# Optimization experiments

Hardware: AMD Instinct MI355X
Metric: run time of the kernel (lower is better)

## Reference

```python
import jax, jax.numpy as jnp
import numpy as np

N = 100000   # nodes
E = 300000   # edges
D = 256      # emb_dim
L = 5        # num_layers
SELF_LOOP_BOND_TYPE = 4
BN_EPS = 1e-5


def setup_inputs() -> dict:
    key = jax.random.key(0)
    ks = jax.random.split(key, 12)
    s = 0.05
    x = jax.random.randint(ks[0], (N, 2), 0, 3)
    edge_index = jax.random.randint(ks[1], (2, E), 0, N)
    edge_attr = jax.random.randint(ks[2], (E, 2), 0, 3)
    x_emb1 = jax.random.normal(ks[3], (120, D), dtype=jnp.float32) * s
    x_emb2 = jax.random.normal(ks[4], (3, D), dtype=jnp.float32) * s
    edge_emb1 = jax.random.normal(ks[5], (L, 6, D), dtype=jnp.float32) * s
    edge_emb2 = jax.random.normal(ks[6], (L, 3, D), dtype=jnp.float32) * s
    W1 = jax.random.normal(ks[7], (L, D, 2 * D), dtype=jnp.float32) * (1.0 / np.sqrt(D))
    b1 = jnp.zeros((L, 2 * D), dtype=jnp.float32)
    W2 = jax.random.normal(ks[8], (L, 2 * D, D), dtype=jnp.float32) * (1.0 / np.sqrt(2 * D))
    b2 = jnp.zeros((L, D), dtype=jnp.float32)
    bn_gamma = jnp.ones((L - 1, D), dtype=jnp.float32)
    bn_beta = jnp.zeros((L - 1, D), dtype=jnp.float32)
    return dict(x=x, edge_index=edge_index, edge_attr=edge_attr,
                x_emb1=x_emb1, x_emb2=x_emb2,
                edge_emb1=edge_emb1, edge_emb2=edge_emb2,
                W1=W1, b1=b1, W2=W2, b2=b2,
                bn_gamma=bn_gamma, bn_beta=bn_beta)


def reference(x, edge_index, edge_attr, x_emb1, x_emb2, edge_emb1, edge_emb2,
              W1, b1, W2, b2, bn_gamma, bn_beta):
    n = x.shape[0]
    loop = jnp.arange(n)
    # add_self_loops: append (i, i) for every node
    src = jnp.concatenate([edge_index[0], loop])  # [E+N]
    dst = jnp.concatenate([edge_index[1], loop])  # [E+N]
    # self-loop edge_attr = (bond_type=4, direction=0)
    self_attr = jnp.concatenate([
        jnp.full((n, 1), SELF_LOOP_BOND_TYPE, dtype=edge_attr.dtype),
        jnp.zeros((n, 1), dtype=edge_attr.dtype)], axis=1)
    ea = jnp.concatenate([edge_attr, self_attr], axis=0)  # [E+N, 2]

    out = x_emb1[x[:, 0]] + x_emb2[x[:, 1]]  # [N, D]
    for l in range(L):
        e_emb = edge_emb1[l][ea[:, 0]] + edge_emb2[l][ea[:, 1]]  # [E+N, D]
        msg = out[src] + e_emb                                   # gather + message
        agg = jax.ops.segment_sum(msg, dst, num_segments=n)      # scatter-add
        h = jax.nn.relu(agg @ W1[l] + b1[l]) @ W2[l] + b2[l]     # GIN MLP
        if l < L - 1:
            mean = h.mean(axis=0)
            var = h.var(axis=0)  # biased var, matches torch BN training
            h = (h - mean) * jax.lax.rsqrt(var + BN_EPS) * bn_gamma[l] + bn_beta[l]
            h = jax.nn.relu(h)
        out = h
    return out
```

## Files before the change

### kernel.cpp

```cpp
#include <hip/hip_runtime.h>

typedef unsigned short u16;
typedef unsigned int u32;

#define DD 256

typedef short  s16x8 __attribute__((ext_vector_type(8)));
typedef short  s16x4 __attribute__((ext_vector_type(4)));
typedef float  f32x4 __attribute__((ext_vector_type(4)));

__device__ __forceinline__ float b2f(u16 u){
  union { u32 i; float f; } c; c.i = ((u32)u) << 16; return c.f;
}
__device__ __forceinline__ u16 f2b(float f){
  union { float f; u32 i; } c; c.f = f;
  u32 b = c.i + 0x7FFFu + ((c.i >> 16) & 1u);
  return (u16)(b >> 16);
}

__global__ void NodeEncoder_72971494359603_kernel(){}

__global__ void probe_dtype(const u32* w, u32* flag){
  if (threadIdx.x == 0 && blockIdx.x == 0){
    int cnt = 0;
    for (int i = 0; i < 256; i++){
      u32 low = w[i] & 0xFFFFu;
      u32 e = (low >> 7) & 0xFFu;
      if (e >= 0x60u && e <= 0x7Eu) cnt++;
    }
    *flag = (cnt >= 192) ? 1u : 0u;
  }
}

__global__ void cvt_in(const void* src, u16* dst, int n, const u32* flag){
  int i = blockIdx.x * 256 + threadIdx.x;
  if (i < n){
    if (*flag){
      dst[i] = ((const u16*)src)[i];
    } else {
      dst[i] = f2b(((const float*)src)[i]);
    }
  }
}

__global__ void store_out(const u16* h, void* dout, int n, const u32* flag){
  int i = blockIdx.x * 256 + threadIdx.x;
  if (i < n){
    if (*flag){
      ((u16*)dout)[i] = h[i];
    } else {
      ((float*)dout)[i] = b2f(h[i]);
    }
  }
}

__global__ void zero_int(int* p, int n){
  int i = blockIdx.x * 256 + threadIdx.x;
  if (i < n) p[i] = 0;
}

__global__ void build_table(const u16* ee1, const u16* ee2, float* TBL){
  int b = blockIdx.x;
  int l = b / 18, c = b % 18, a = c / 3, bb = c % 3;
  int j = threadIdx.x;
  TBL[b * DD + j] = b2f(ee1[(l * 6 + a) * DD + j]) + b2f(ee2[(l * 3 + bb) * DD + j]);
}

__global__ void hist_kernel(const int* dst, int* counts, int E){
  int e = blockIdx.x * 256 + threadIdx.x;
  if (e < E) atomicAdd(&counts[dst[e]], 1);
}

__global__ void scan_sums(const int* counts, int* bsum, int N){
  __shared__ int red[256];
  int tid = threadIdx.x;
  int base = blockIdx.x * 1024;
  int s = 0;
  for (int i = tid; i < 1024; i += 256){
    int g = base + i;
    if (g < N) s += counts[g];
  }
  red[tid] = s;
  __syncthreads();
  for (int off = 128; off > 0; off >>= 1){
    if (tid < off) red[tid] += red[tid + off];
    __syncthreads();
  }
  if (tid == 0) bsum[blockIdx.x] = red[0];
}

__global__ void scan_top(int* bsum, int nb){
  if (threadIdx.x == 0 && blockIdx.x == 0){
    int acc = 0;
    for (int i = 0; i < nb; i++){ int t = bsum[i]; bsum[i] = acc; acc += t; }
  }
}

__global__ void scan_block(const int* counts, const int* bsum,
                           int* offsets, int* cursor, int N){
  __shared__ int tsum[256];
  int b = blockIdx.x;
  int tid = threadIdx.x;
  int base = b * 1024;
  int v0, v1, v2, v3;
  int g = base + tid * 4;
  v0 = (g + 0 < N) ? counts[g + 0] : 0;
  v1 = (g + 1 < N) ? counts[g + 1] : 0;
  v2 = (g + 2 < N) ? counts[g + 2] : 0;
  v3 = (g + 3 < N) ? counts[g + 3] : 0;
  tsum[tid] = v0 + v1 + v2 + v3;
  __syncthreads();
  for (int off = 1; off < 256; off <<= 1){
    int t = (tid >= off) ? tsum[tid - off] : 0;
    __syncthreads();
    tsum[tid] += t;
    __syncthreads();
  }
  int excl = (tid == 0 ? 0 : tsum[tid - 1]) + bsum[b];
  if (g + 0 < N){ offsets[g + 0] = excl; cursor[g + 0] = excl; } excl += v0;
  if (g + 1 < N){ offsets[g + 1] = excl; cursor[g + 1] = excl; } excl += v1;
  if (g + 2 < N){ offsets[g + 2] = excl; cursor[g + 2] = excl; } excl += v2;
  if (g + 3 < N){ offsets[g + 3] = excl; cursor[g + 3] = excl; }
}

__global__ void fill_csr(const int* ei, const int* ea, int* cursor,
                         int* payload, int E){
  int e = blockIdx.x * 256 + threadIdx.x;
  if (e < E){
    int d = ei[E + e];
    int pos = atomicAdd(&cursor[d], 1);
    int a = ea[2 * e], bb = ea[2 * e + 1];
    payload[pos] = ei[e] | ((a * 3 + bb) << 17);
  }
}

__global__ void node_embed(const int* x, const u16* xe1, const u16* xe2,
                           u16* out, int N){
  int idx = blockIdx.x * 256 + threadIdx.x;
  if (idx < N * DD){
    int n = idx >> 8, j = idx & 255;
    int x0 = x[2 * n], x1 = x[2 * n + 1];
    out[idx] = f2b(b2f(xe1[x0 * DD + j]) + b2f(xe2[x1 * DD + j]));
  }
}

__global__ void aggregate(const u16* __restrict__ feat, const float* __restrict__ TBL,
                          const int* __restrict__ offsets, const int* __restrict__ counts,
                          const int* __restrict__ payload, u16* __restrict__ agg, int N,
                          const float* __restrict__ sums, const u16* __restrict__ gamma,
                          const u16* __restrict__ beta, float invN, int apply_bn){
  __shared__ __align__(16) float T[18 * DD];
  int tid = threadIdx.x;
  for (int i = tid; i < 18 * DD; i += 256) T[i] = TBL[i];
  __syncthreads();
  int wave = tid >> 6, lane = tid & 63;
  int c4 = lane * 4;
  float sc[4], sh[4];
  if (apply_bn){
#pragma unroll
    for (int e = 0; e < 4; e++){
      int j = c4 + e;
      float mean = sums[j] * invN;
      float var = sums[DD + j] * invN - mean * mean;
      if (var < 0.f) var = 0.f;
      float scl = rsqrtf(var + 1e-5f) * b2f(gamma[j]);
      sc[e] = scl; sh[e] = b2f(beta[j]) - mean * scl;
    }
  } else {
#pragma unroll
    for (int e = 0; e < 4; e++){ sc[e] = 1.f; sh[e] = 0.f; }
  }
  int n0 = blockIdx.x * 32 + wave * 8;
  for (int u = 0; u < 8; u++){
    int n = n0 + u;
    if (n >= N) return;
    s16x4 sv = *(const s16x4*)(feat + (size_t)n * DD + c4);
    f32x4 tb = *(const f32x4*)(T + 12 * DD + c4);
    float v0 = b2f((u16)sv[0]) * sc[0] + sh[0];
    float v1 = b2f((u16)sv[1]) * sc[1] + sh[1];
    float v2 = b2f((u16)sv[2]) * sc[2] + sh[2];
    float v3 = b2f((u16)sv[3]) * sc[3] + sh[3];
    if (apply_bn){
      v0 = fmaxf(v0, 0.f); v1 = fmaxf(v1, 0.f);
      v2 = fmaxf(v2, 0.f); v3 = fmaxf(v3, 0.f);
    }
    float a0 = v0 + tb[0], a1 = v1 + tb[1], a2 = v2 + tb[2], a3 = v3 + tb[3];
    int e0 = offsets[n], cnt = counts[n];
    for (int e = e0; e < e0 + cnt; e++){
      int pl = payload[e];
      int src = pl & 0x1FFFF;
      int idx = pl >> 17;
      s16x4 rv = *(const s16x4*)(feat + (size_t)src * DD + c4);
      f32x4 tv = *(const f32x4*)(T + idx * DD + c4);
      float w0 = b2f((u16)rv[0]) * sc[0] + sh[0];
      float w1 = b2f((u16)rv[1]) * sc[1] + sh[1];
      float w2 = b2f((u16)rv[2]) * sc[2] + sh[2];
      float w3 = b2f((u16)rv[3]) * sc[3] + sh[3];
      if (apply_bn){
        w0 = fmaxf(w0, 0.f); w1 = fmaxf(w1, 0.f);
        w2 = fmaxf(w2, 0.f); w3 = fmaxf(w3, 0.f);
      }
      a0 += w0 + tv[0];
      a1 += w1 + tv[1];
      a2 += w2 + tv[2];
      a3 += w3 + tv[3];
    }
    s16x4 o;
    o[0] = (short)f2b(a0); o[1] = (short)f2b(a1);
    o[2] = (short)f2b(a2); o[3] = (short)f2b(a3);
    *(s16x4*)(agg + (size_t)n * DD + c4) = o;
  }
}

__global__ void pack_B(const u16* __restrict__ W, u16* __restrict__ Wp, int K, int Nc){
  int idx = blockIdx.x * 256 + threadIdx.x;
  int lane = idx & 63;
  int t = idx >> 6;
  int nk = K >> 5;
  int ksub = t % nk, cblk = t / nk;
  if (cblk >= (Nc >> 4)) return;
  int col = cblk * 16 + (lane & 15);
  int krow = ksub * 32 + (lane >> 4) * 8;
  u16* dst = Wp + (size_t)idx * 8;
#pragma unroll
  for (int e = 0; e < 8; e++)
    dst[e] = W[(size_t)(krow + e) * Nc + col];
}

__global__ void mlp_fused(const u16* __restrict__ A, const u16* __restrict__ Wp1,
                          const u16* __restrict__ bias1, const u16* __restrict__ Wp2,
                          const u16* __restrict__ bias2, u16* __restrict__ H, int M){
  __shared__ __align__(16) u16 As[64 * 256];
  __shared__ __align__(16) u16 Ms[64 * 128];
  int tid = threadIdx.x;
  int lane = tid & 63;
  int wave = tid >> 6;
  int wr = wave >> 2, wc = wave & 3;
  int row0 = blockIdx.x * 64;
  int lrow = lane & 15;
  int lk8 = (lane >> 4) * 8;
  int r4 = (lane >> 4) * 4;

  int srow = tid >> 5, slot = tid & 31;
#pragma unroll
  for (int p = 0; p < 4; p++){
    int r = p * 16 + srow;
    int gr = row0 + r; if (gr > M - 1) gr = M - 1;
    s16x8 v = *(const s16x8*)(A + (size_t)gr * DD + slot * 8);
    int byteo = r * 512 + ((slot * 16) ^ ((r & 7) << 4));
    *(s16x8*)((char*)As + byteo) = v;
  }

  f32x4 zero = {0.f, 0.f, 0.f, 0.f};
  f32x4 acc2[2][4];
#pragma unroll
  for (int m = 0; m < 2; m++)
#pragma unroll
    for (int n = 0; n < 4; n++) acc2[m][n] = zero;

  __syncthreads();

  for (int c = 0; c < 4; c++){
    f32x4 acc1[2][2];
#pragma unroll
    for (int m = 0; m < 2; m++)
#pragma unroll
      for (int n = 0; n < 2; n++) acc1[m][n] = zero;
#pragma unroll
    for (int ks = 0; ks < 8; ks++){
      s16x8 af[2], bf[2];
#pragma unroll
      for (int m = 0; m < 2; m++){
        int arow = wr * 32 + m * 16 + lrow;
        int byteo = arow * 512 + (((ks * 32 + lk8) * 2) ^ ((arow & 7) << 4));
        af[m] = *(const s16x8*)((const char*)As + byteo);
      }
#pragma unroll
      for (int n = 0; n < 2; n++){
        int cb = c * 8 + wc * 2 + n;
        size_t fidx = ((size_t)cb * 8 + ks) * 64 + lane;
        bf[n] = *(const s16x8*)(Wp1 + fidx * 8);
      }
#pragma unroll
      for (int m = 0; m < 2; m++)
#pragma unroll
        for (int n = 0; n < 2; n++)
          acc1[m][n] = __builtin_amdgcn_mfma_f32_16x16x32_bf16(
              af[m], bf[n], acc1[m][n], 0, 0, 0);
    }
    __syncthreads();
#pragma unroll
    for (int n = 0; n < 2; n++){
      float bv = b2f(bias1[c * 128 + wc * 32 + n * 16 + lrow]);
      int colb = (wc * 32 + n * 16 + lrow) * 2;
#pragma unroll
      for (int m = 0; m < 2; m++){
#pragma unroll
        for (int r = 0; r < 4; r++){
          float v = acc1[m][n][r] + bv;
          if (v < 0.f) v = 0.f;
          int mrow = wr * 32 + m * 16 + r4 + r;
          int byteo = (mrow * 256 + colb) ^ ((mrow & 7) << 4);
          *(u16*)((char*)Ms + byteo) = f2b(v);
        }
      }
    }
    __syncthreads();
#pragma unroll
    for (int ks = 0; ks < 4; ks++){
      s16x8 mf[2], wf[4];
#pragma unroll
      for (int m = 0; m < 2; m++){
        int mrow = wr * 32 + m * 16 + lrow;
        int byteo = mrow * 256 + (((ks * 32 + lk8) * 2) ^ ((mrow & 7) << 4));
        mf[m] = *(const s16x8*)((const char*)Ms + byteo);
      }
#pragma unroll
      for (int n = 0; n < 4; n++){
        int cb2 = wc * 4 + n;
        size_t fidx = ((size_t)cb2 * 16 + c * 4 + ks) * 64 + lane;
        wf[n] = *(const s16x8*)(Wp2 + fidx * 8);
      }
#pragma unroll
      for (int m = 0; m < 2; m++)
#pragma unroll
        for (int n = 0; n < 4; n++)
          acc2[m][n] = __builtin_amdgcn_mfma_f32_16x16x32_bf16(
              mf[m], wf[n], acc2[m][n], 0, 0, 0);
    }
  }

  float bv2[4];
#pragma unroll
  for (int n = 0; n < 4; n++) bv2[n] = b2f(bias2[wc * 64 + n * 16 + lrow]);
#pragma unroll
  for (int m = 0; m < 2; m++){
    int rb = row0 + wr * 32 + m * 16 + r4;
#pragma unroll
    for (int r = 0; r < 4; r++){
      int row = rb + r;
      if (row >= M) continue;
      u16* cp = H + (size_t)row * DD + wc * 64 + lrow;
#pragma unroll
      for (int n = 0; n < 4; n++)
        cp[n * 16] = f2b(acc2[m][n][r] + bv2[n]);
    }
  }
}

#define SBLK 256
__global__ void bn_stats(const u16* __restrict__ h, float* __restrict__ partial,
                         int N, int rpb){
  __shared__ float redS[8][256];
  __shared__ float redQ[8][256];
  int t = threadIdx.x;
  int rl = t >> 5, cg = (t & 31) * 8;
  int r0 = blockIdx.x * rpb;
  int r1 = r0 + rpb; if (r1 > N) r1 = N;
  float s[8], q[8];
#pragma unroll
  for (int e = 0; e < 8; e++){ s[e] = 0.f; q[e] = 0.f; }
  for (int r = r0 + rl; r < r1; r += 8){
    s16x8 v = *(const s16x8*)(h + (size_t)r * DD + cg);
#pragma unroll
    for (int e = 0; e < 8; e++){
      float f = b2f((u16)v[e]);
      s[e] += f; q[e] += f * f;
    }
  }
#pragma unroll
  for (int e = 0; e < 8; e++){ redS[rl][cg + e] = s[e]; redQ[rl][cg + e] = q[e]; }
  __syncthreads();
  float a = 0.f, b = 0.f;
#pragma unroll
  for (int k = 0; k < 8; k++){ a += redS[k][t]; b += redQ[k][t]; }
  partial[(size_t)blockIdx.x * DD + t] = a;
  partial[(size_t)(SBLK + blockIdx.x) * DD + t] = b;
}

__global__ void bn_reduce(const float* __restrict__ partial, float* __restrict__ sums){
  int j = threadIdx.x;
  int which = blockIdx.x;
  float s = 0.f;
  for (int i = 0; i < SBLK; i++)
    s += partial[(size_t)(which * SBLK + i) * DD + j];
  sums[which * DD + j] = s;
}

extern "C" void kernel_launch(void* const* d_in, const int* in_sizes, int n_in,
                              void* d_out, int out_size, void* d_ws, size_t ws_size,
                              hipStream_t stream){
  (void)n_in; (void)out_size; (void)ws_size;
  const int* x    = (const int*)d_in[0];
  const int* ei   = (const int*)d_in[1];
  const int* ea   = (const int*)d_in[2];
  const void* xe1 = d_in[3];
  const void* xe2 = d_in[4];
  const void* ee1 = d_in[5];
  const void* ee2 = d_in[6];
  const void* W1  = d_in[7];
  const void* b1  = d_in[8];
  const void* W2  = d_in[9];
  const void* b2  = d_in[10];
  const void* gam = d_in[11];
  const void* bet = d_in[12];

  int N = in_sizes[0] / 2;
  int E = in_sizes[1] / 2;
  int NB = (N + 1023) / 1024;
  const int L = 5;

  char* base = (char*)d_ws;
  size_t off = 0;
  u32* flag    = (u32*)(base + off);   off += 256;
  float* TBL   = (float*)(base + off); off += ((size_t)L * 18 * DD * 4 + 255) & ~(size_t)255;
  int* counts  = (int*)(base + off);   off += ((size_t)N * 4 + 255) & ~(size_t)255;
  int* offsets = (int*)(base + off);   off += ((size_t)N * 4 + 255) & ~(size_t)255;
  int* cursor  = (int*)(base + off);   off += ((size_t)N * 4 + 255) & ~(size_t)255;
  int* bsum    = (int*)(base + off);   off += ((size_t)NB * 4 + 255) & ~(size_t)255;
  int* payload = (int*)(base + off);   off += ((size_t)E * 4 + 255) & ~(size_t)255;
  float* part  = (float*)(base + off); off += ((size_t)2 * SBLK * DD * 4 + 255) & ~(size_t)255;
  float* sums  = (float*)(base + off); off += ((size_t)2 * DD * 4 + 255) & ~(size_t)255;
  u16* wx1  = (u16*)(base + off); off += ((size_t)120 * DD * 2 + 255) & ~(size_t)255;
  u16* wx2  = (u16*)(base + off); off += ((size_t)3 * DD * 2 + 255) & ~(size_t)255;
  u16* wee1 = (u16*)(base + off); off += ((size_t)L * 6 * DD * 2 + 255) & ~(size_t)255;
  u16* wee2 = (u16*)(base + off); off += ((size_t)L * 3 * DD * 2 + 255) & ~(size_t)255;
  u16* wW1  = (u16*)(base + off); off += ((size_t)L * DD * 2 * DD * 2 + 255) & ~(size_t)255;
  u16* wb1  = (u16*)(base + off); off += ((size_t)L * 2 * DD * 2 + 255) & ~(size_t)255;
  u16* wW2  = (u16*)(base + off); off += ((size_t)L * 2 * DD * DD * 2 + 255) & ~(size_t)255;
  u16* wb2  = (u16*)(base + off); off += ((size_t)L * DD * 2 + 255) & ~(size_t)255;
  u16* wgam = (u16*)(base + off); off += ((size_t)(L - 1) * DD * 2 + 255) & ~(size_t)255;
  u16* wbet = (u16*)(base + off); off += ((size_t)(L - 1) * DD * 2 + 255) & ~(size_t)255;
  u16* Wp1  = (u16*)(base + off); off += ((size_t)L * DD * 2 * DD * 2 + 255) & ~(size_t)255;
  u16* Wp2  = (u16*)(base + off); off += ((size_t)L * 2 * DD * DD * 2 + 255) & ~(size_t)255;
  u16* feat = (u16*)(base + off); off += ((size_t)N * DD * 2 + 255) & ~(size_t)255;
  u16* agg  = (u16*)(base + off); off += ((size_t)N * DD * 2 + 255) & ~(size_t)255;

  probe_dtype<<<1, 64, 0, stream>>>((const u32*)xe1, flag);
  cvt_in<<<(120 * DD + 255) / 256, 256, 0, stream>>>(xe1, wx1, 120 * DD, flag);
  cvt_in<<<(3 * DD + 255) / 256, 256, 0, stream>>>(xe2, wx2, 3 * DD, flag);
  cvt_in<<<(L * 6 * DD + 255) / 256, 256, 0, stream>>>(ee1, wee1, L * 6 * DD, flag);
  cvt_in<<<(L * 3 * DD + 255) / 256, 256, 0, stream>>>(ee2, wee2, L * 3 * DD, flag);
  cvt_in<<<(L * DD * 2 * DD + 255) / 256, 256, 0, stream>>>(W1, wW1, L * DD * 2 * DD, flag);
  cvt_in<<<(L * 2 * DD + 255) / 256, 256, 0, stream>>>(b1, wb1, L * 2 * DD, flag);
  cvt_in<<<(L * 2 * DD * DD + 255) / 256, 256, 0, stream>>>(W2, wW2, L * 2 * DD * DD, flag);
  cvt_in<<<(L * DD + 255) / 256, 256, 0, stream>>>(b2, wb2, L * DD, flag);
  cvt_in<<<((L - 1) * DD + 255) / 256, 256, 0, stream>>>(gam, wgam, (L - 1) * DD, flag);
  cvt_in<<<((L - 1) * DD + 255) / 256, 256, 0, stream>>>(bet, wbet, (L - 1) * DD, flag);

  build_table<<<90, 256, 0, stream>>>(wee1, wee2, TBL);
  for (int l = 0; l < L; l++){
    pack_B<<<64, 256, 0, stream>>>(wW1 + (size_t)l * DD * 2 * DD,
                                   Wp1 + (size_t)l * DD * 2 * DD, DD, 2 * DD);
    pack_B<<<64, 256, 0, stream>>>(wW2 + (size_t)l * 2 * DD * DD,
                                   Wp2 + (size_t)l * 2 * DD * DD, 2 * DD, DD);
  }
  zero_int<<<(N + 255) / 256, 256, 0, stream>>>(counts, N);
  hist_kernel<<<(E + 255) / 256, 256, 0, stream>>>(ei + E, counts, E);
  scan_sums<<<NB, 256, 0, stream>>>(counts, bsum, N);
  scan_top<<<1, 64, 0, stream>>>(bsum, NB);
  scan_block<<<NB, 256, 0, stream>>>(counts, bsum, offsets, cursor, N);
  fill_csr<<<(E + 255) / 256, 256, 0, stream>>>(ei, ea, cursor, payload, E);

  node_embed<<<(N * DD + 255) / 256, 256, 0, stream>>>(x, wx1, wx2, feat, N);

  int rpb_s = (N + SBLK - 1) / SBLK;
  float invN = 1.0f / (float)N;

  for (int l = 0; l < L; l++){
    aggregate<<<(N + 31) / 32, 256, 0, stream>>>(
        feat, TBL + (size_t)l * 18 * DD, offsets, counts, payload, agg, N,
        sums, wgam + (size_t)(l > 0 ? l - 1 : 0) * DD,
        wbet + (size_t)(l > 0 ? l - 1 : 0) * DD, invN, l > 0 ? 1 : 0);

    mlp_fused<<<(N + 63) / 64, 512, 0, stream>>>(
        agg, Wp1 + (size_t)l * DD * 2 * DD, wb1 + (size_t)l * 2 * DD,
        Wp2 + (size_t)l * 2 * DD * DD, wb2 + (size_t)l * DD, feat, N);

    if (l < L - 1){
      bn_stats<<<SBLK, 256, 0, stream>>>(feat, part, N, rpb_s);
      bn_reduce<<<2, 256, 0, stream>>>(part, sums);
    }
  }

  store_out<<<(N * DD + 255) / 256, 256, 0, stream>>>(feat, d_out, N * DD, flag);
}
```

Baseline: 1.574 ms.

## Restructure fused MLP per-wave and fold BN statistics into its epilogue

The MLP kernel now gives each wave its own 32-row tile with private LDS, so the block-wide syncthreads disappear, and each wave computes all 256 output columns across 16 hidden chunks. The output is staged through LDS for coalesced 16-byte stores, and per-column sum and sum-of-squares partials are accumulated in the same pass. This removes the separate bn_stats kernel and its full re-read of the feature matrix. bn_reduce is widened to 16 blocks with shuffle reductions to handle the larger number of partials. The trade-off is a large accumulator footprint (128 fp32 per lane for acc2), lower occupancy, and weight fragments being re-fetched from global memory per wave without reuse across waves.

```diff
diff --git a/kernel.cpp b/kernel.cpp
--- a/kernel.cpp
+++ b/kernel.cpp
@@ -227,40 +227,36 @@
     dst[e] = W[(size_t)(krow + e) * Nc + col];
 }
 
-__global__ void mlp_fused(const u16* __restrict__ A, const u16* __restrict__ Wp1,
-                          const u16* __restrict__ bias1, const u16* __restrict__ Wp2,
-                          const u16* __restrict__ bias2, u16* __restrict__ H, int M){
-  __shared__ __align__(16) u16 As[64 * 256];
-  __shared__ __align__(16) u16 Ms[64 * 128];
-  int tid = threadIdx.x;
-  int lane = tid & 63;
-  int wave = tid >> 6;
-  int wr = wave >> 2, wc = wave & 3;
-  int row0 = blockIdx.x * 64;
-  int lrow = lane & 15;
-  int lk8 = (lane >> 4) * 8;
-  int r4 = (lane >> 4) * 4;
-
-  int srow = tid >> 5, slot = tid & 31;
-#pragma unroll
-  for (int p = 0; p < 4; p++){
-    int r = p * 16 + srow;
-    int gr = row0 + r; if (gr > M - 1) gr = M - 1;
-    s16x8 v = *(const s16x8*)(A + (size_t)gr * DD + slot * 8);
-    int byteo = r * 512 + ((slot * 16) ^ ((r & 7) << 4));
-    *(s16x8*)((char*)As + byteo) = v;
+__global__ __launch_bounds__(256, 2)
+void mlp_fused(const u16* __restrict__ A, const u16* __restrict__ Wp1,
+               const u16* __restrict__ bias1, const u16* __restrict__ Wp2,
+               const u16* __restrict__ bias2, u16* __restrict__ H,
+               float* __restrict__ partial, int npart, int M){
+  __shared__ __align__(16) u16 As[4 * 32 * 256];
+  __shared__ __align__(16) u16 Ms[4 * 32 * 64];
+  int tid = threadIdx.x, lane = tid & 63, wave = tid >> 6;
+  char* as = (char*)(As + wave * 32 * 256);
+  char* ms = (char*)(Ms + wave * 32 * 64);
+  int wrow0 = blockIdx.x * 128 + wave * 32;
+  int lr = lane & 15, hi = lane >> 4;
+
+#pragma unroll
+  for (int p = 0; p < 16; p++){
+    int lin = p * 64 + lane;
+    int r = lin >> 5, sl = lin & 31;
+    int gr = wrow0 + r; if (gr > M - 1) gr = M - 1;
+    s16x8 v = *(const s16x8*)(A + (size_t)gr * DD + sl * 8);
+    *(s16x8*)(as + r * 512 + ((sl << 4) ^ ((r & 7) << 4))) = v;
   }
 
   f32x4 zero = {0.f, 0.f, 0.f, 0.f};
-  f32x4 acc2[2][4];
+  f32x4 acc2[2][16];
 #pragma unroll
   for (int m = 0; m < 2; m++)
 #pragma unroll
-    for (int n = 0; n < 4; n++) acc2[m][n] = zero;
-
-  __syncthreads();
-
-  for (int c = 0; c < 4; c++){
+    for (int n = 0; n < 16; n++) acc2[m][n] = zero;
+
+  for (int cc = 0; cc < 16; cc++){
     f32x4 acc1[2][2];
 #pragma unroll
     for (int m = 0; m < 2; m++)
@@ -268,123 +264,114 @@
       for (int n = 0; n < 2; n++) acc1[m][n] = zero;
 #pragma unroll
     for (int ks = 0; ks < 8; ks++){
-      s16x8 af[2], bf[2];
+      s16x8 af[2];
 #pragma unroll
       for (int m = 0; m < 2; m++){
-        int arow = wr * 32 + m * 16 + lrow;
-        int byteo = arow * 512 + (((ks * 32 + lk8) * 2) ^ ((arow & 7) << 4));
-        af[m] = *(const s16x8*)((const char*)As + byteo);
+        int arow = m * 16 + lr;
+        af[m] = *(const s16x8*)(as + arow * 512 +
+                                ((ks * 64 + hi * 16) ^ ((arow & 7) << 4)));
       }
 #pragma unroll
       for (int n = 0; n < 2; n++){
-        int cb = c * 8 + wc * 2 + n;
-        size_t fidx = ((size_t)cb * 8 + ks) * 64 + lane;
-        bf[n] = *(const s16x8*)(Wp1 + fidx * 8);
-      }
-#pragma unroll
-      for (int m = 0; m < 2; m++)
-#pragma unroll
-        for (int n = 0; n < 2; n++)
-          acc1[m][n] = __builtin_amdgcn_mfma_f32_16x16x32_bf16(
-              af[m], bf[n], acc1[m][n], 0, 0, 0);
-    }
-    __syncthreads();
+        int cb = cc * 2 + n;
+        s16x8 bf = *(const s16x8*)(Wp1 + (((size_t)cb * 8 + ks) * 64 + lane) * 8);
+        acc1[0][n] = __builtin_amdgcn_mfma_f32_16x16x32_bf16(af[0], bf, acc1[0][n], 0, 0, 0);
+        acc1[1][n] = __builtin_amdgcn_mfma_f32_16x16x32_bf16(af[1], bf, acc1[1][n], 0, 0, 0);
+      }
+    }
 #pragma unroll
     for (int n = 0; n < 2; n++){
-      float bv = b2f(bias1[c * 128 + wc * 32 + n * 16 + lrow]);
-      int colb = (wc * 32 + n * 16 + lrow) * 2;
+      float bv = b2f(bias1[cc * 32 + n * 16 + lr]);
+      int c2 = (n * 16 + lr) * 2;
 #pragma unroll
       for (int m = 0; m < 2; m++){
 #pragma unroll
         for (int r = 0; r < 4; r++){
+          int mrow = m * 16 + hi * 4 + r;
           float v = acc1[m][n][r] + bv;
-          if (v < 0.f) v = 0.f;
-          int mrow = wr * 32 + m * 16 + r4 + r;
-          int byteo = (mrow * 256 + colb) ^ ((mrow & 7) << 4);
-          *(u16*)((char*)Ms + byteo) = f2b(v);
+          v = fmaxf(v, 0.f);
+          *(u16*)(ms + mrow * 128 + (c2 ^ ((mrow & 7) << 4))) = f2b(v);
         }
       }
     }
-    __syncthreads();
-#pragma unroll
-    for (int ks = 0; ks < 4; ks++){
-      s16x8 mf[2], wf[4];
-#pragma unroll
-      for (int m = 0; m < 2; m++){
-        int mrow = wr * 32 + m * 16 + lrow;
-        int byteo = mrow * 256 + (((ks * 32 + lk8) * 2) ^ ((mrow & 7) << 4));
-        mf[m] = *(const s16x8*)((const char*)Ms + byteo);
-      }
-#pragma unroll
-      for (int n = 0; n < 4; n++){
-        int cb2 = wc * 4 + n;
-        size_t fidx = ((size_t)cb2 * 16 + c * 4 + ks) * 64 + lane;
-        wf[n] = *(const s16x8*)(Wp2 + fidx * 8);
-      }
-#pragma unroll
-      for (int m = 0; m < 2; m++)
-#pragma unroll
-        for (int n = 0; n < 4; n++)
-          acc2[m][n] = __builtin_amdgcn_mfma_f32_16x16x32_bf16(
-              mf[m], wf[n], acc2[m][n], 0, 0, 0);
-    }
-  }
-
-  float bv2[4];
-#pragma unroll
-  for (int n = 0; n < 4; n++) bv2[n] = b2f(bias2[wc * 64 + n * 16 + lrow]);
-#pragma unroll
-  for (int m = 0; m < 2; m++){
-    int rb = row0 + wr * 32 + m * 16 + r4;
-#pragma unroll
-    for (int r = 0; r < 4; r++){
-      int row = rb + r;
-      if (row >= M) continue;
-      u16* cp = H + (size_t)row * DD + wc * 64 + lrow;
-#pragma unroll
-      for (int n = 0; n < 4; n++)
-        cp[n * 16] = f2b(acc2[m][n][r] + bv2[n]);
-    }
-  }
-}
-
-#define SBLK 256
-__global__ void bn_stats(const u16* __restrict__ h, float* __restrict__ partial,
-                         int N, int rpb){
-  __shared__ float redS[8][256];
-  __shared__ float redQ[8][256];
+    s16x8 mf[2];
+#pragma unroll
+    for (int m = 0; m < 2; m++){
+      int mrow = m * 16 + lr;
+      mf[m] = *(const s16x8*)(ms + mrow * 128 + ((hi * 16) ^ ((mrow & 7) << 4)));
+    }
+#pragma unroll
+    for (int n = 0; n < 16; n++){
+      s16x8 wf = *(const s16x8*)(Wp2 + (((size_t)n * 16 + cc) * 64 + lane) * 8);
+      acc2[0][n] = __builtin_amdgcn_mfma_f32_16x16x32_bf16(mf[0], wf, acc2[0][n], 0, 0, 0);
+      acc2[1][n] = __builtin_amdgcn_mfma_f32_16x16x32_bf16(mf[1], wf, acc2[1][n], 0, 0, 0);
+    }
+  }
+
+#pragma unroll
+  for (int n = 0; n < 16; n++){
+    float bv = b2f(bias2[n * 16 + lr]);
+    int c2 = (n * 16 + lr) * 2;
+#pragma unroll
+    for (int m = 0; m < 2; m++){
+#pragma unroll
+      for (int r = 0; r < 4; r++){
+        int mrow = m * 16 + hi * 4 + r;
+        float v = acc2[m][n][r] + bv;
+        *(u16*)(as + mrow * 512 + (c2 ^ ((mrow & 7) << 4))) = f2b(v);
+      }
+    }
+  }
+
+  float s[8], q[8];
+#pragma unroll
+  for (int e = 0; e < 8; e++){ s[e] = 0.f; q[e] = 0.f; }
+  int sl = lane & 31;
+#pragma unroll
+  for (int p = 0; p < 16; p++){
+    int lin = p * 64 + lane;
+    int r = lin >> 5;
+    s16x8 v = *(const s16x8*)(as + r * 512 + ((sl << 4) ^ ((r & 7) << 4)));
+    int gr = wrow0 + r;
+    if (gr < M){
+      *(s16x8*)(H + (size_t)gr * DD + sl * 8) = v;
+      if (partial){
+#pragma unroll
+        for (int e = 0; e < 8; e++){
+          float f = b2f((u16)v[e]);
+          s[e] += f; q[e] += f * f;
+        }
+      }
+    }
+  }
+  if (partial){
+#pragma unroll
+    for (int e = 0; e < 8; e++){
+      s[e] += __shfl_xor(s[e], 32);
+      q[e] += __shfl_xor(q[e], 32);
+    }
+    if (lane < 32){
+      int pidx = blockIdx.x * 4 + wave;
+#pragma unroll
+      for (int e = 0; e < 8; e++){
+        partial[(size_t)pidx * DD + sl * 8 + e] = s[e];
+        partial[(size_t)(npart + pidx) * DD + sl * 8 + e] = q[e];
+      }
+    }
+  }
+}
+
+__global__ void bn_reduce(const float* __restrict__ partial, float* __restrict__ sums,
+                          int npart){
+  int b = blockIdx.x, which = b >> 3, jg = b & 7;
   int t = threadIdx.x;
-  int rl = t >> 5, cg = (t & 31) * 8;
-  int r0 = blockIdx.x * rpb;
-  int r1 = r0 + rpb; if (r1 > N) r1 = N;
-  float s[8], q[8];
-#pragma unroll
-  for (int e = 0; e < 8; e++){ s[e] = 0.f; q[e] = 0.f; }
-  for (int r = r0 + rl; r < r1; r += 8){
-    s16x8 v = *(const s16x8*)(h + (size_t)r * DD + cg);
-#pragma unroll
-    for (int e = 0; e < 8; e++){
-      float f = b2f((u16)v[e]);
-      s[e] += f; q[e] += f * f;
-    }
-  }
-#pragma unroll
-  for (int e = 0; e < 8; e++){ redS[rl][cg + e] = s[e]; redQ[rl][cg + e] = q[e]; }
-  __syncthreads();
-  float a = 0.f, b = 0.f;
-#pragma unroll
-  for (int k = 0; k < 8; k++){ a += redS[k][t]; b += redQ[k][t]; }
-  partial[(size_t)blockIdx.x * DD + t] = a;
-  partial[(size_t)(SBLK + blockIdx.x) * DD + t] = b;
-}
-
-__global__ void bn_reduce(const float* __restrict__ partial, float* __restrict__ sums){
-  int j = threadIdx.x;
-  int which = blockIdx.x;
+  int j = jg * 32 + (t >> 3);
+  int li = t & 7;
   float s = 0.f;
-  for (int i = 0; i < SBLK; i++)
-    s += partial[(size_t)(which * SBLK + i) * DD + j];
-  sums[which * DD + j] = s;
+  for (int i = li; i < npart; i += 8)
+    s += partial[(size_t)(which * npart + i) * DD + j];
+  s += __shfl_xor(s, 1); s += __shfl_xor(s, 2); s += __shfl_xor(s, 4);
+  if (li == 0) sums[which * DD + j] = s;
 }
 
 extern "C" void kernel_launch(void* const* d_in, const int* in_sizes, int n_in,
@@ -409,6 +396,8 @@
   int E = in_sizes[1] / 2;
   int NB = (N + 1023) / 1024;
   const int L = 5;
+  int nblkm = (N + 127) / 128;
+  int npart = nblkm * 4;
 
   char* base = (char*)d_ws;
   size_t off = 0;
@@ -419,7 +408,7 @@
   int* cursor  = (int*)(base + off);   off += ((size_t)N * 4 + 255) & ~(size_t)255;
   int* bsum    = (int*)(base + off);   off += ((size_t)NB * 4 + 255) & ~(size_t)255;
   int* payload = (int*)(base + off);   off += ((size_t)E * 4 + 255) & ~(size_t)255;
-  float* part  = (float*)(base + off); off += ((size_t)2 * SBLK * DD * 4 + 255) & ~(size_t)255;
+  float* part  = (float*)(base + off); off += ((size_t)2 * npart * DD * 4 + 255) & ~(size_t)255;
   float* sums  = (float*)(base + off); off += ((size_t)2 * DD * 4 + 255) & ~(size_t)255;
   u16* wx1  = (u16*)(base + off); off += ((size_t)120 * DD * 2 + 255) & ~(size_t)255;
   u16* wx2  = (u16*)(base + off); off += ((size_t)3 * DD * 2 + 255) & ~(size_t)255;
@@ -464,7 +453,6 @@
 
   node_embed<<<(N * DD + 255) / 256, 256, 0, stream>>>(x, wx1, wx2, feat, N);
 
-  int rpb_s = (N + SBLK - 1) / SBLK;
   float invN = 1.0f / (float)N;
 
   for (int l = 0; l < L; l++){
@@ -473,13 +461,13 @@
         sums, wgam + (size_t)(l > 0 ? l - 1 : 0) * DD,
         wbet + (size_t)(l > 0 ? l - 1 : 0) * DD, invN, l > 0 ? 1 : 0);
 
-    mlp_fused<<<(N + 63) / 64, 512, 0, stream>>>(
+    mlp_fused<<<nblkm, 256, 0, stream>>>(
         agg, Wp1 + (size_t)l * DD * 2 * DD, wb1 + (size_t)l * 2 * DD,
-        Wp2 + (size_t)l * 2 * DD * DD, wb2 + (size_t)l * DD, feat, N);
+        Wp2 + (size_t)l * 2 * DD * DD, wb2 + (size_t)l * DD, feat,
+        (l < L - 1) ? part : (float*)nullptr, npart, N);
 
     if (l < L - 1){
-      bn_stats<<<SBLK, 256, 0, stream>>>(feat, part, N, rpb_s);
-      bn_reduce<<<2, 256, 0, stream>>>(part, sums);
+      bn_reduce<<<16, 256, 0, stream>>>(part, sums, npart);
     }
   }
 
```

Result: slower. 2.631 ms (+67.1%).
